# Kernel optimization log

Hardware: AMD Instinct MI355X
Metric: run time of the kernel (lower is better)

Reference implementation:

```python
import jax, jax.numpy as jnp
import numpy as np

N = 100000
E = 1600000
D_IN = 128
D_OUT = 128

def setup_inputs() -> dict:
    key = jax.random.key(0)
    k1, k2, k3, k4, k5, k6 = jax.random.split(key, 6)
    h = jax.random.normal(k1, (N, D_IN), dtype=jnp.float32)
    # norm ~ deg^{-1/2}; use positive uniform values as stand-in
    norm = jax.random.uniform(k2, (N, 1), dtype=jnp.float32, minval=0.05, maxval=1.0)
    src = jax.random.randint(k3, (E,), 0, N, dtype=jnp.int32)
    dst = jax.random.randint(k4, (E,), 0, N, dtype=jnp.int32)
    weight = jax.random.normal(k5, (D_IN, D_OUT), dtype=jnp.float32) * (2.0 / (D_IN + D_OUT)) ** 0.5
    bias = jnp.zeros((D_OUT,), dtype=jnp.float32)
    return {"h": h, "norm": norm, "src": src, "dst": dst, "weight": weight, "bias": bias}

def reference(h, norm, src, dst, weight, bias):
    n_nodes = h.shape[0]
    hw = h @ weight                      # [N, D_out] dense GEMM
    hw = hw * norm                       # pre-aggregation degree scale
    msgs = hw[src]                       # gather: [E, D_out]
    agg = jax.ops.segment_sum(msgs, dst, num_segments=n_nodes)  # scatter-sum
    out = agg * norm + bias              # post-scale + bias
    return out
```

## Files before the change

### kernel.cpp

```cpp
#include <hip/hip_runtime.h>
#include <hip/hip_bf16.h>

#define D 128
#define D4 32
#define CHUNK 6144
#define MAXB 2048
#define NSEG 8
#define SL 4096

typedef __attribute__((ext_vector_type(8))) short bf16x8;
typedef __attribute__((ext_vector_type(8))) unsigned short ushort8;
typedef __attribute__((ext_vector_type(4))) float f32x4;

static __device__ __forceinline__ unsigned short f2bf(float f) {
    unsigned u = __float_as_uint(f);
    u += 0x7FFFu + ((u >> 16) & 1u);
    return (unsigned short)(u >> 16);
}
static __device__ __forceinline__ float bf2f(unsigned short u) {
    return __uint_as_float(((unsigned)u) << 16);
}

__global__ __launch_bounds__(256) void wcvt_kernel(
    const float* __restrict__ W, unsigned short* __restrict__ Wt)
{
    const int idx = blockIdx.x * 256 + threadIdx.x;
    const float4 w = ((const float4*)W)[idx];
    const int k = idx >> 5;
    const int c = (idx & 31) * 4;
    Wt[(c + 0) * 128 + k] = f2bf(w.x);
    Wt[(c + 1) * 128 + k] = f2bf(w.y);
    Wt[(c + 2) * 128 + k] = f2bf(w.z);
    Wt[(c + 3) * 128 + k] = f2bf(w.w);
}

__global__ __launch_bounds__(512) void gemm_mfma_kernel(
    const float* __restrict__ h, const unsigned short* __restrict__ Wt,
    const float* __restrict__ norm, unsigned short* __restrict__ hwb,
    int n_nodes)
{
    __shared__ unsigned short Bs[128 * 136];

    const int t = threadIdx.x;
    const int row0 = blockIdx.x * 128;

    #pragma unroll
    for (int i = 0; i < 4; ++i) {
        const int idx = t + 512 * i;
        const int c = idx >> 4;
        const int k8 = idx & 15;
        *(ushort8*)&Bs[c * 136 + k8 * 8] = ((const ushort8*)Wt)[idx];
    }
    __syncthreads();

    const int wv = t >> 6;
    const int lane = t & 63;
    const int m = lane & 15;
    const int quad = lane >> 4;

    long gra = row0 + wv * 16 + m;
    if (gra >= n_nodes) gra = n_nodes - 1;
    const float* hrow = h + gra * D;

    f32x4 acc[8];
    #pragma unroll
    for (int nt = 0; nt < 8; ++nt) { f32x4 z = {0.f, 0.f, 0.f, 0.f}; acc[nt] = z; }

    #pragma unroll
    for (int kt = 0; kt < 4; ++kt) {
        const float4 a0 = *(const float4*)(hrow + kt * 32 + quad * 8);
        const float4 a1 = *(const float4*)(hrow + kt * 32 + quad * 8 + 4);
        bf16x8 af;
        unsigned short* ap = (unsigned short*)&af;
        ap[0] = f2bf(a0.x); ap[1] = f2bf(a0.y); ap[2] = f2bf(a0.z); ap[3] = f2bf(a0.w);
        ap[4] = f2bf(a1.x); ap[5] = f2bf(a1.y); ap[6] = f2bf(a1.z); ap[7] = f2bf(a1.w);
        #pragma unroll
        for (int nt = 0; nt < 8; ++nt) {
            const bf16x8 bfr = *(const bf16x8*)&Bs[(nt * 16 + m) * 136 + kt * 32 + quad * 8];
            acc[nt] = __builtin_amdgcn_mfma_f32_16x16x32_bf16(af, bfr, acc[nt], 0, 0, 0);
        }
    }

    float nv[4];
    #pragma unroll
    for (int i = 0; i < 4; ++i) {
        const int gr = row0 + wv * 16 + quad * 4 + i;
        nv[i] = (gr < n_nodes) ? norm[gr] : 0.f;
    }

    __syncthreads();
    #pragma unroll
    for (int nt = 0; nt < 8; ++nt) {
        #pragma unroll
        for (int i = 0; i < 4; ++i) {
            const int r = wv * 16 + quad * 4 + i;
            Bs[r * 136 + nt * 16 + m] = f2bf(acc[nt][i] * nv[i]);
        }
    }
    __syncthreads();

    #pragma unroll
    for (int i2 = 0; i2 < 4; ++i2) {
        const int idx = t + 512 * i2;
        const int r = idx >> 4;
        const int c8 = idx & 15;
        const int gr = row0 + r;
        if (gr < n_nodes)
            *(ushort8*)&hwb[(size_t)gr * D + c8 * 8] =
                *(const ushort8*)&Bs[r * 136 + c8 * 8];
    }
}

__global__ __launch_bounds__(1024) void hist_kernel(
    const int* __restrict__ dst, int* __restrict__ H,
    unsigned short* __restrict__ hwb, int n_edges, int n_nodes)
{
    __shared__ int lbh[MAXB];
    const int t = threadIdx.x;
    const int g = blockIdx.x;
    for (int i = t; i < MAXB; i += 1024) lbh[i] = 0;
    if (g == 0 && t < 32) {
        ushort4 z; z.x = z.y = z.z = z.w = 0;
        ((ushort4*)(hwb + (size_t)n_nodes * D))[t] = z;
    }
    __syncthreads();
    const int e0 = g * CHUNK;
    const int e1 = min(e0 + CHUNK, n_edges);
    for (int e = e0 + t; e < e1; e += 1024) {
        atomicAdd(&lbh[dst[e] >> 6], 1);
    }
    __syncthreads();
    for (int i = t; i < MAXB; i += 1024) {
        H[(size_t)g * MAXB + i] = lbh[i];
    }
}

__global__ __launch_bounds__(256) void chunkscan_local_kernel(
    const int* __restrict__ H, int* __restrict__ CO, int* __restrict__ PS,
    int eb)
{
    const int b = blockIdx.x * 256 + threadIdx.x;
    const int seg = blockIdx.y;
    const int glen = (eb + NSEG - 1) / NSEG;
    const int g0 = seg * glen;
    const int g1 = min(g0 + glen, eb);
    int run = 0;
    for (int g = g0; g < g1; ++g) {
        CO[(size_t)g * MAXB + b] = run;
        run += H[(size_t)g * MAXB + b];
    }
    PS[seg * MAXB + b] = run;
}

__global__ __launch_bounds__(256) void bucket_scan_kernel(
    const int* __restrict__ PS, int* __restrict__ boff, int* __restrict__ SB)
{
    __shared__ int tmp[256];
    const int t = threadIdx.x;
    int v[8];
    int s = 0;
    #pragma unroll
    for (int k = 0; k < 8; ++k) {
        const int i = t * 8 + k;
        int c = 0;
        #pragma unroll
        for (int sg = 0; sg < NSEG; ++sg) c += PS[sg * MAXB + i];
        v[k] = c; s += c;
    }
    tmp[t] = s;
    __syncthreads();
    for (int ofs = 1; ofs < 256; ofs <<= 1) {
        int x = (t >= ofs) ? tmp[t - ofs] : 0;
        __syncthreads();
        tmp[t] += x;
        __syncthreads();
    }
    int run = tmp[t] - s;
    #pragma unroll
    for (int k = 0; k < 8; ++k) {
        const int i = t * 8 + k;
        boff[i] = run;
        int sb = run;
        #pragma unroll
        for (int sg = 0; sg < NSEG; ++sg) {
            SB[sg * MAXB + i] = sb;
            sb += PS[sg * MAXB + i];
        }
        run += v[k];
    }
    if (t == 255) boff[MAXB] = run;
}

__global__ __launch_bounds__(1024) void bscatter_kernel(
    const int* __restrict__ src, const int* __restrict__ dst,
    const int* __restrict__ CO, const int* __restrict__ SB,
    unsigned int* __restrict__ ebuf, int n_edges, int eb)
{
    __shared__ int lbh[MAXB];
    __shared__ int lofs[MAXB];
    const int t = threadIdx.x;
    const int g = blockIdx.x;
    const int glen = (eb + NSEG - 1) / NSEG;
    const int seg = g / glen;
    for (int i = t; i < MAXB; i += 1024) {
        lbh[i] = 0;
        lofs[i] = SB[seg * MAXB + i] + CO[(size_t)g * MAXB + i];
    }
    __syncthreads();
    const int e0 = g * CHUNK;
    const int e1 = min(e0 + CHUNK, n_edges);
    for (int e = e0 + t; e < e1; e += 1024) {
        const int d = dst[e];
        const int bk = d >> 6;
        const int r = atomicAdd(&lbh[bk], 1);
        ebuf[lofs[bk] + r] = (unsigned)src[e] | ((unsigned)(d & 63) << 17);
    }
}

__global__ __launch_bounds__(256) void fillagg_kernel(
    const unsigned int* __restrict__ ebuf, const int* __restrict__ boff,
    int* __restrict__ srcs_g, const unsigned short* __restrict__ hwb,
    const float* __restrict__ norm, const float* __restrict__ bias,
    float* __restrict__ out, int n_nodes)
{
    __shared__ int slds[SL];
    __shared__ int lcnt[64];
    __shared__ int lcur[64];
    __shared__ int loff[64];
    const int t = threadIdx.x;
    const int b = blockIdx.x;
    const int gn0 = b * 64;

    if (t < 64) lcnt[t] = 0;
    __syncthreads();
    const int w0 = boff[b], w1 = boff[b + 1];
    const int wlen = w1 - w0;
    const bool uselds = (wlen + 480) <= SL;
    const int gbase = w0 + 448 * b;

    for (int e = w0 + t; e < w1; e += 256) {
        atomicAdd(&lcnt[(ebuf[e] >> 17) & 63], 1);
    }
    __syncthreads();
    if (t < 64) {
        const int c = lcnt[t];
        const int p = (c + 7) & ~7;
        int x = p;
        #pragma unroll
        for (int ofs = 1; ofs < 64; ofs <<= 1) {
            const int y = __shfl_up(x, ofs, 64);
            if (t >= ofs) x += y;
        }
        const int base = x - p;
        lcur[t] = base;
        loff[t] = base;
    }
    __syncthreads();
    for (int e = w0 + t; e < w1; e += 256) {
        const unsigned rec = ebuf[e];
        const int loc = (rec >> 17) & 63;
        const int pos = atomicAdd(&lcur[loc], 1);
        const int sv = (int)(rec & 0x1FFFFu);
        if (uselds) slds[pos] = sv; else srcs_g[gbase + pos] = sv;
    }
    for (int w = t; w < 512; w += 256) {
        const int ln = w >> 3, k = w & 7;
        const int gn = gn0 + ln;
        if (gn < n_nodes) {
            const int c = lcnt[ln];
            const int pad = (8 - (c & 7)) & 7;
            if (k < pad) {
                const int pos = loff[ln] + c + k;
                if (uselds) slds[pos] = n_nodes; else srcs_g[gbase + pos] = n_nodes;
            }
        }
    }
    __syncthreads();

    const ushort4* hw4 = (const ushort4*)hwb;
    const int grp = t >> 5;
    const int l = t & 31;
    const float4 bs = ((const float4*)bias)[l];
    for (int nn = 0; nn < 8; ++nn) {
        const int loc = grp * 8 + nn;
        const int gn = gn0 + loc;
        if (gn >= n_nodes) continue;
        const int start = loff[loc];
        const int deg = lcnt[loc];
        const int nb8 = (deg + 7) >> 3;
        float4 acc; acc.x = acc.y = acc.z = acc.w = 0.f;
        int myidx = 0;
        for (int bb = 0; bb < nb8; ++bb) {
            const int q = bb & 3;
            if (q == 0) {
                const int ri = start + bb * 8 + l;
                myidx = uselds ? slds[ri] : srcs_g[gbase + ri];
            }
            ushort4 v[8];
            #pragma unroll
            for (int jj = 0; jj < 8; ++jj) {
                const int s = __shfl(myidx, q * 8 + jj, 32);
                v[jj] = hw4[(long)s * D4 + l];
            }
            #pragma unroll
            for (int jj = 0; jj < 8; ++jj) {
                acc.x += bf2f(v[jj].x);
                acc.y += bf2f(v[jj].y);
                acc.z += bf2f(v[jj].z);
                acc.w += bf2f(v[jj].w);
            }
        }
        const float nv = norm[gn];
        float4 o;
        o.x = acc.x * nv + bs.x;
        o.y = acc.y * nv + bs.y;
        o.z = acc.z * nv + bs.z;
        o.w = acc.w * nv + bs.w;
        ((float4*)out)[(long)gn * D4 + l] = o;
    }
}

__global__ __launch_bounds__(256) void scatter_kernel(
    const unsigned short* __restrict__ hwb, const int* __restrict__ src,
    const int* __restrict__ dst, float* __restrict__ out, int n_edges)
{
    const int idx = blockIdx.x * 256 + threadIdx.x;
    if (idx >= n_edges * D4) return;
    const int e = idx >> 5;
    const int g = idx & 31;
    const int s = src[e];
    const int d = dst[e];
    const ushort4 v = ((const ushort4*)hwb)[(long)s * D4 + g];
    float* o = out + (long)d * D + g * 4;
    atomicAdd(o + 0, bf2f(v.x));
    atomicAdd(o + 1, bf2f(v.y));
    atomicAdd(o + 2, bf2f(v.z));
    atomicAdd(o + 3, bf2f(v.w));
}

__global__ __launch_bounds__(256) void finalize_kernel(
    float* __restrict__ out, const float* __restrict__ norm,
    const float* __restrict__ bias, int n_nodes)
{
    const int idx = blockIdx.x * 256 + threadIdx.x;
    if (idx >= n_nodes * D4) return;
    const int n = idx >> 5;
    const int g = idx & 31;
    float4 v = ((float4*)out)[idx];
    const float nv = norm[n];
    const float4 b = ((const float4*)bias)[g];
    v.x = v.x * nv + b.x;
    v.y = v.y * nv + b.y;
    v.z = v.z * nv + b.z;
    v.w = v.w * nv + b.w;
    ((float4*)out)[idx] = v;
}

extern "C" void kernel_launch(void* const* d_in, const int* in_sizes, int n_in,
                              void* d_out, int out_size, void* d_ws, size_t ws_size,
                              hipStream_t stream) {
    const float* h    = (const float*)d_in[0];
    const float* norm = (const float*)d_in[1];
    const int*   src  = (const int*)d_in[2];
    const int*   dst  = (const int*)d_in[3];
    const float* W    = (const float*)d_in[4];
    const float* bias = (const float*)d_in[5];
    float* out = (float*)d_out;

    const int n_nodes = in_sizes[1];
    const int n_edges = in_sizes[2];

    const int NBUCK = (n_nodes + 63) >> 6;
    const int EB    = (n_edges + CHUNK - 1) / CHUNK;
    const int srcs_len = n_edges + 448 * NBUCK + 64;

    size_t p = 0;
    auto take = [&](size_t bytes) {
        size_t cur = p;
        p += (bytes + 255) & ~(size_t)255;
        return cur;
    };
    const size_t hwb_off  = take(((size_t)n_nodes + 1) * D * sizeof(unsigned short));
    const size_t wt_off   = take((size_t)D * D * sizeof(unsigned short));
    const size_t srcs_off = take((size_t)srcs_len * sizeof(int));
    const size_t ebuf_off = take((size_t)n_edges * sizeof(unsigned int));
    const size_t boff_off = take((MAXB + 1) * sizeof(int));
    const size_t H_off    = take((size_t)EB * MAXB * sizeof(int));
    const size_t PS_off   = take((size_t)NSEG * MAXB * sizeof(int));
    const size_t SB_off   = take((size_t)NSEG * MAXB * sizeof(int));
    const size_t CO_off   = take((size_t)EB * MAXB * sizeof(int));
    const size_t needed = p;

    char* ws = (char*)d_ws;
    unsigned short* hwb = (unsigned short*)(ws + hwb_off);
    unsigned short* Wt  = (unsigned short*)(ws + wt_off);

    wcvt_kernel<<<16, 256, 0, stream>>>(W, Wt);
    gemm_mfma_kernel<<<(n_nodes + 127) / 128, 512, 0, stream>>>(h, Wt, norm, hwb, n_nodes);

    if (ws_size >= needed && NBUCK <= MAXB && n_nodes <= 131072 && EB <= 1024) {
        int* srcs  = (int*)(ws + srcs_off);
        unsigned int* ebuf = (unsigned int*)(ws + ebuf_off);
        int* boff  = (int*)(ws + boff_off);
        int* H     = (int*)(ws + H_off);
        int* PS    = (int*)(ws + PS_off);
        int* SBp   = (int*)(ws + SB_off);
        int* CO    = (int*)(ws + CO_off);

        hist_kernel<<<EB, 1024, 0, stream>>>(dst, H, hwb, n_edges, n_nodes);
        chunkscan_local_kernel<<<dim3(MAXB / 256, NSEG), 256, 0, stream>>>(H, CO, PS, EB);
        bucket_scan_kernel<<<1, 256, 0, stream>>>(PS, boff, SBp);
        bscatter_kernel<<<EB, 1024, 0, stream>>>(src, dst, CO, SBp, ebuf, n_edges, EB);
        fillagg_kernel<<<NBUCK, 256, 0, stream>>>(ebuf, boff, srcs, hwb, norm, bias,
                                                  out, n_nodes);
    } else {
        hipMemsetAsync(d_out, 0, (size_t)out_size * sizeof(float), stream);
        const int work = n_edges * D4;
        scatter_kernel<<<(work + 255) / 256, 256, 0, stream>>>(hwb, src, dst, out, n_edges);
        const int work2 = n_nodes * D4;
        finalize_kernel<<<(work2 + 255) / 256, 256, 0, stream>>>(out, norm, bias, n_nodes);
    }
}
```

Before: 235.4 us.

## Fuse edge-sort pipeline into one cooperative kernel with grid syncs

Replaces the five separate launches (histogram, chunk scan, bucket scan, bucket scatter, fill+aggregate) with a single cooperative kernel that separates the phases with grid.sync(). It also raises CHUNK so the edge-block count stays small enough for every block to be co-resident. The aim is to remove launch gaps and per-kernel ramp-up. The cost is that the aggregation phase now runs on only EB blocks of 1024 threads, far fewer than the earlier NBUCK-sized grid, and grid-wide barriers can serialise work.

```diff
diff --git a/kernel.cpp b/kernel.cpp
--- a/kernel.cpp
+++ b/kernel.cpp
@@ -1,9 +1,12 @@
 #include <hip/hip_runtime.h>
 #include <hip/hip_bf16.h>
+#include <hip/hip_cooperative_groups.h>
+
+namespace cg = cooperative_groups;
 
 #define D 128
 #define D4 32
-#define CHUNK 6144
+#define CHUNK 6400
 #define MAXB 2048
 #define NSEG 8
 #define SL 4096
@@ -108,6 +111,207 @@
         if (gr < n_nodes)
             *(ushort8*)&hwb[(size_t)gr * D + c8 * 8] =
                 *(const ushort8*)&Bs[r * 136 + c8 * 8];
+    }
+}
+
+__global__ __launch_bounds__(1024) void coop_edge_kernel(
+    const int* __restrict__ src, const int* __restrict__ dst,
+    int* __restrict__ H, int* __restrict__ PS, int* __restrict__ SB,
+    int* __restrict__ boff, int* __restrict__ CO,
+    unsigned int* __restrict__ ebuf, int* __restrict__ srcs_g,
+    const unsigned short* __restrict__ hwb,
+    const float* __restrict__ norm, const float* __restrict__ bias,
+    float* __restrict__ out,
+    int n_edges, int n_nodes, int EB, int NBUCK)
+{
+    __shared__ int smem[SL + 192];
+
+    cg::grid_group grid = cg::this_grid();
+    const int t = threadIdx.x;
+    const int g = blockIdx.x;
+    const int gid = g * 1024 + t;
+    const int glen = (EB + NSEG - 1) / NSEG;
+    const int e0 = g * CHUNK;
+    const int e1 = min(e0 + CHUNK, n_edges);
+
+    {
+        int* lbh = smem;
+        for (int i = t; i < MAXB; i += 1024) lbh[i] = 0;
+        if (g == 0 && t < 32) {
+            ushort4 z; z.x = z.y = z.z = z.w = 0;
+            ((ushort4*)(hwb + (size_t)n_nodes * D))[t] = z;
+        }
+        __syncthreads();
+        for (int e = e0 + t; e < e1; e += 1024)
+            atomicAdd(&lbh[dst[e] >> 6], 1);
+        __syncthreads();
+        for (int i = t; i < MAXB; i += 1024) H[(size_t)g * MAXB + i] = lbh[i];
+    }
+    grid.sync();
+
+    if (gid < NSEG * MAXB) {
+        const int seg = gid >> 11;
+        const int c = gid & (MAXB - 1);
+        const int g0 = seg * glen, g1 = min(g0 + glen, EB);
+        int s = 0;
+        for (int gg = g0; gg < g1; ++gg) s += H[(size_t)gg * MAXB + c];
+        PS[seg * MAXB + c] = s;
+    }
+    grid.sync();
+
+    if (g == 0) {
+        int* tmp = smem;
+        const int cA = 2 * t, cB = 2 * t + 1;
+        int va = 0, vb = 0;
+        #pragma unroll
+        for (int sg = 0; sg < NSEG; ++sg) { va += PS[sg * MAXB + cA]; vb += PS[sg * MAXB + cB]; }
+        tmp[t] = va + vb;
+        __syncthreads();
+        for (int ofs = 1; ofs < 1024; ofs <<= 1) {
+            const int x = (t >= ofs) ? tmp[t - ofs] : 0;
+            __syncthreads();
+            tmp[t] += x;
+            __syncthreads();
+        }
+        const int run = tmp[t] - (va + vb);
+        boff[cA] = run;
+        boff[cB] = run + va;
+        if (t == 1023) boff[MAXB] = tmp[1023];
+        int sb = run;
+        #pragma unroll
+        for (int sg = 0; sg < NSEG; ++sg) { SB[sg * MAXB + cA] = sb; sb += PS[sg * MAXB + cA]; }
+        sb = run + va;
+        #pragma unroll
+        for (int sg = 0; sg < NSEG; ++sg) { SB[sg * MAXB + cB] = sb; sb += PS[sg * MAXB + cB]; }
+    }
+    grid.sync();
+
+    if (gid < NSEG * MAXB) {
+        const int seg = gid >> 11;
+        const int c = gid & (MAXB - 1);
+        const int g0 = seg * glen, g1 = min(g0 + glen, EB);
+        int run = SB[seg * MAXB + c];
+        for (int gg = g0; gg < g1; ++gg) {
+            CO[(size_t)gg * MAXB + c] = run;
+            run += H[(size_t)gg * MAXB + c];
+        }
+    }
+    grid.sync();
+
+    {
+        int* lbh = smem;
+        int* lofs = smem + MAXB;
+        for (int i = t; i < MAXB; i += 1024) {
+            lbh[i] = 0;
+            lofs[i] = CO[(size_t)g * MAXB + i];
+        }
+        __syncthreads();
+        for (int e = e0 + t; e < e1; e += 1024) {
+            const int d = dst[e];
+            const int bk = d >> 6;
+            const int r = atomicAdd(&lbh[bk], 1);
+            ebuf[lofs[bk] + r] = (unsigned)src[e] | ((unsigned)(d & 63) << 17);
+        }
+    }
+    grid.sync();
+
+    {
+        int* slds = smem;
+        int* lcnt = smem + SL;
+        int* lcur = smem + SL + 64;
+        int* loff = smem + SL + 128;
+        const ushort4* hw4 = (const ushort4*)hwb;
+        const int grp = t >> 5;
+        const int l = t & 31;
+        const float4 bs = ((const float4*)bias)[l];
+
+        for (int bkt = g; bkt < NBUCK; bkt += gridDim.x) {
+            __syncthreads();
+            if (t < 64) lcnt[t] = 0;
+            __syncthreads();
+            const int w0 = boff[bkt], w1 = boff[bkt + 1];
+            const int wlen = w1 - w0;
+            const bool uselds = (wlen + 480) <= SL;
+            const int gbase = w0 + 448 * bkt;
+            const int gn0 = bkt * 64;
+
+            for (int e = w0 + t; e < w1; e += 1024)
+                atomicAdd(&lcnt[(ebuf[e] >> 17) & 63], 1);
+            __syncthreads();
+            if (t < 64) {
+                const int c = lcnt[t];
+                const int p = (c + 7) & ~7;
+                int x = p;
+                #pragma unroll
+                for (int ofs = 1; ofs < 64; ofs <<= 1) {
+                    const int y = __shfl_up(x, ofs, 64);
+                    if (t >= ofs) x += y;
+                }
+                const int base = x - p;
+                lcur[t] = base;
+                loff[t] = base;
+            }
+            __syncthreads();
+            for (int e = w0 + t; e < w1; e += 1024) {
+                const unsigned rec = ebuf[e];
+                const int loc = (rec >> 17) & 63;
+                const int pos = atomicAdd(&lcur[loc], 1);
+                const int sv = (int)(rec & 0x1FFFFu);
+                if (uselds) slds[pos] = sv; else srcs_g[gbase + pos] = sv;
+            }
+            for (int w = t; w < 512; w += 1024) {
+                const int ln = w >> 3, k = w & 7;
+                const int gn = gn0 + ln;
+                if (gn < n_nodes) {
+                    const int c = lcnt[ln];
+                    const int pad = (8 - (c & 7)) & 7;
+                    if (k < pad) {
+                        const int pos = loff[ln] + c + k;
+                        if (uselds) slds[pos] = n_nodes; else srcs_g[gbase + pos] = n_nodes;
+                    }
+                }
+            }
+            __syncthreads();
+
+            #pragma unroll
+            for (int nn = 0; nn < 2; ++nn) {
+                const int loc = grp * 2 + nn;
+                const int gn = gn0 + loc;
+                if (gn >= n_nodes) continue;
+                const int start = loff[loc];
+                const int deg = lcnt[loc];
+                const int nb8 = (deg + 7) >> 3;
+                float4 acc; acc.x = acc.y = acc.z = acc.w = 0.f;
+                int myidx = 0;
+                for (int bb = 0; bb < nb8; ++bb) {
+                    const int q = bb & 3;
+                    if (q == 0) {
+                        const int ri = start + bb * 8 + l;
+                        myidx = uselds ? slds[ri] : srcs_g[gbase + ri];
+                    }
+                    ushort4 v[8];
+                    #pragma unroll
+                    for (int jj = 0; jj < 8; ++jj) {
+                        const int s = __shfl(myidx, q * 8 + jj, 32);
+                        v[jj] = hw4[(long)s * D4 + l];
+                    }
+                    #pragma unroll
+                    for (int jj = 0; jj < 8; ++jj) {
+                        acc.x += bf2f(v[jj].x);
+                        acc.y += bf2f(v[jj].y);
+                        acc.z += bf2f(v[jj].z);
+                        acc.w += bf2f(v[jj].w);
+                    }
+                }
+                const float nv = norm[gn];
+                float4 o;
+                o.x = acc.x * nv + bs.x;
+                o.y = acc.y * nv + bs.y;
+                o.z = acc.z * nv + bs.z;
+                o.w = acc.w * nv + bs.w;
+                ((float4*)out)[(long)gn * D4 + l] = o;
+            }
+        }
     }
 }
 
@@ -398,7 +602,41 @@
     wcvt_kernel<<<16, 256, 0, stream>>>(W, Wt);
     gemm_mfma_kernel<<<(n_nodes + 127) / 128, 512, 0, stream>>>(h, Wt, norm, hwb, n_nodes);
 
-    if (ws_size >= needed && NBUCK <= MAXB && n_nodes <= 131072 && EB <= 1024) {
+    static int s_max_coop_blocks = -1;
+    if (s_max_coop_blocks < 0) {
+        int nb = 0;
+        if (hipOccupancyMaxActiveBlocksPerMultiprocessor(&nb, coop_edge_kernel, 1024, 0)
+            != hipSuccess) nb = 0;
+        int dev = 0;
+        hipGetDevice(&dev);
+        int ncu = 0;
+        if (hipDeviceGetAttribute(&ncu, hipDeviceAttributeMultiprocessorCount, dev)
+            != hipSuccess) ncu = 0;
+        s_max_coop_blocks = nb * ncu;
+    }
+
+    const bool ws_ok = (ws_size >= needed) && (NBUCK <= MAXB) && (n_nodes <= 131072);
+    const bool coop_ok = ws_ok && EB >= 16 && EB <= 512 && EB <= s_max_coop_blocks;
+
+    if (coop_ok) {
+        int* srcs  = (int*)(ws + srcs_off);
+        unsigned int* ebuf = (unsigned int*)(ws + ebuf_off);
+        int* boff  = (int*)(ws + boff_off);
+        int* H     = (int*)(ws + H_off);
+        int* PS    = (int*)(ws + PS_off);
+        int* SBp   = (int*)(ws + SB_off);
+        int* CO    = (int*)(ws + CO_off);
+
+        int ne = n_edges, nn = n_nodes, eb = EB, nbk = NBUCK;
+        void* args[] = {
+            (void*)&src, (void*)&dst, (void*)&H, (void*)&PS, (void*)&SBp,
+            (void*)&boff, (void*)&CO, (void*)&ebuf, (void*)&srcs, (void*)&hwb,
+            (void*)&norm, (void*)&bias, (void*)&out,
+            (void*)&ne, (void*)&nn, (void*)&eb, (void*)&nbk
+        };
+        hipLaunchCooperativeKernel((void*)coop_edge_kernel, dim3(EB), dim3(1024),
+                                   args, 0, stream);
+    } else if (ws_ok && EB <= 1024) {
         int* srcs  = (int*)(ws + srcs_off);
         unsigned int* ebuf = (unsigned int*)(ws + ebuf_off);
         int* boff  = (int*)(ws + boff_off);
```

After: 227.4 us. 3.4% less time.
